# Performance work log

Measured on AMD Instinct MI355X. Metric: run time of the kernel, lower is better.

The kernel has to match this reference:

```python
import jax, jax.numpy as jnp
import numpy as np

D_MODEL, N, L_MAX, BATCH = 512, 64, 2048, 8


def _make_s4_buffers(n):
    # HiPPO-NPLR: hippo[i,j] = sqrt(2i+1)sqrt(2j+1) if i>j; i+1 if i==j (1-indexed)
    i = np.arange(1, n + 1)
    row = np.sqrt(2 * i + 1.0)
    hippo = np.tril(np.outer(row, row), -1) + np.diag(i + 1.0)
    p = 0.5 * np.sqrt(2 * i + 1.0)
    q = 2.0 * p
    S = -hippo + np.outer(p, q)
    lam, V = np.linalg.eig(S)
    Vc = V.conj().T
    return Vc @ p, Vc @ q, lam  # complex128 -> cast to complex64 later


def setup_inputs() -> dict:
    key = jax.random.key(0)
    k1, k2, k3, k4 = jax.random.split(key, 4)
    xavier_std = float(np.sqrt(2.0 / (N + D_MODEL)))
    p, q, lam = _make_s4_buffers(N)
    u = jax.random.normal(k1, (BATCH, L_MAX, D_MODEL), jnp.float32)
    B = jax.random.normal(k2, (D_MODEL, N), jnp.float32) * xavier_std
    Ct = jax.random.normal(k3, (D_MODEL, N), jnp.float32) * xavier_std
    D = jnp.ones((D_MODEL,), jnp.float32)
    log_step = (jax.random.uniform(k4, (D_MODEL,), jnp.float32)
                * (np.log(0.1) - np.log(0.001)) + np.log(0.001))
    return {
        "u": u, "B": B, "Ct": Ct, "D": D, "log_step": log_step,
        "p": jnp.asarray(p, jnp.complex64),
        "q": jnp.asarray(q, jnp.complex64),
        "lam": jnp.asarray(lam, jnp.complex64),
    }


def _s4_forward(u, B, Ct, D, log_step, p, q, lam):
    L = u.shape[1]  # l_max
    omega = jnp.exp((2j * np.pi / L) * jnp.arange(L)).astype(jnp.complex64)  # (L,)
    step = jnp.exp(log_step)                                                 # (d,)
    g = (2.0 / step)[:, None] * ((1.0 - omega) / (1.0 + omega))[None, :]     # (d, L)
    c = 2.0 / (1.0 + omega)                                                  # (L,)
    Bc = B.astype(jnp.complex64)
    Ctc = Ct.astype(jnp.complex64)  # Ct is real -> conj is identity
    v00 = Ctc * Bc                              # (d, n)
    v01 = Ctc * p[None, :]                      # (d, n)
    v10 = jnp.conj(q)[None, :] * Bc             # (d, n)
    v11 = jnp.broadcast_to(jnp.conj(q) * p, v00.shape)
    V = jnp.stack([v00, v01, v10, v11], 0)      # (4, d, n)
    # fused Cauchy reduction: k[k,d,l] = sum_n V[k,d,n] / (g[d,l] - lam[n])
    recip = 1.0 / (g[:, :, None] - lam[None, None, :])  # (d, L, n) big intermediate
    k00, k01, k10, k11 = jnp.einsum('kdn,dln->kdl', V, recip)
    at_roots = c * (k00 - k01 * k10 / (1.0 + k11))      # (d, L)
    # ifft + index reversal (i -> (L - i) mod L), keep real part
    order = (L - jnp.arange(L)) % L
    K = jnp.fft.ifft(at_roots, n=L, axis=-1)[:, order].real.astype(jnp.float32)  # (d, L)
    # non-circular convolution via length-2L FFT
    ud = jnp.fft.rfft(jnp.pad(u, ((0, 0), (0, L), (0, 0))), axis=1)   # (B, L+1, d)
    Kd = jnp.fft.rfft(jnp.pad(K, ((0, 0), (0, L))), axis=-1)          # (d, L+1)
    y = jnp.fft.irfft(jnp.swapaxes(ud, 1, 2) * Kd[None], axis=-1)[..., :L]  # (B, d, L)
    return jnp.swapaxes(y, 1, 2) + D[None, None, :] * u


def reference(u, B, Ct, D, log_step, p, q, lam):
    return _s4_forward(u, B, Ct, D, log_step, p, q, lam)
```

## Files before the change

kernel.cpp:

```cpp
#include <hip/hip_runtime.h>
#include <math.h>

#define D_MODEL 512
#define NSTATE  64
#define LSEQ    2048
#define L2X     4096
#define NBATCH  8
#define NT      512

#define SQ2H 0.70710678118654752f

__device__ __forceinline__ float2 cmulf(float2 a, float2 b) {
    return make_float2(a.x * b.x - a.y * b.y, a.x * b.y + a.y * b.x);
}
__device__ __forceinline__ float2 cmulc(float2 a, float2 w) {
    return make_float2(a.x * w.x + a.y * w.y, a.y * w.x - a.x * w.y);
}
__device__ __forceinline__ float2 cadd(float2 a, float2 b) { return make_float2(a.x + b.x, a.y + b.y); }
__device__ __forceinline__ float2 csub(float2 a, float2 b) { return make_float2(a.x - b.x, a.y - b.y); }
__device__ __forceinline__ float rcpf(float x) { return __builtin_amdgcn_rcpf(x); }
__device__ __forceinline__ float2 cdiv_fast(float2 a, float2 b) {
    float inv = rcpf(b.x * b.x + b.y * b.y);
    return make_float2((a.x * b.x + a.y * b.y) * inv, (a.y * b.x - a.x * b.y) * inv);
}
__device__ __forceinline__ int finitef(float v) {
    return (v == v) && (v < 3.0e38f) && (v > -3.0e38f);
}
__device__ __forceinline__ int octrev12(int x) {
    return ((x & 7) << 9) | ((x & 0x38) << 3) | ((x >> 3) & 0x38) | ((x >> 9) & 7);
}

__device__ __forceinline__ int tidx(int i) { return i + (i >> 4); }
__device__ __forceinline__ int kswz(int i) { return i ^ (i >> 6); }

#define TW_SZ  1088
#define BUF_SZ 4352

__device__ __forceinline__ float2 twget4(const float2* tw, int k) {
    float2 w = tw[tidx(k & 1023)];
    if (k & 1024) w = make_float2(w.y, -w.x);
    if (k & 2048) w = make_float2(-w.x, -w.y);
    return w;
}
#define A4096 (-1.5339807878856412e-3f)
__device__ __forceinline__ void build_tw(float2* tw) {
    for (int k = threadIdx.x; k < 1024; k += NT) {
        float s, c;
        sincosf(A4096 * (float)k, &s, &c);
        tw[tidx(k)] = make_float2(c, s);
    }
}

__device__ __forceinline__ float2 ldc(const float* f, int n, int mode) {
    if (mode == 0) return make_float2(f[n], 0.0f);
    if (mode == 1) return make_float2(f[n], f[64 + n]);
    return make_float2(f[2 * n], f[2 * n + 1]);
}

__device__ __forceinline__ void dft4f(float2 a, float2 b, float2 c, float2 d, float2* F) {
    float2 t0 = cadd(a, c), t1 = csub(a, c);
    float2 t2 = cadd(b, d), t3 = csub(b, d);
    F[0] = cadd(t0, t2);
    F[1] = make_float2(t1.x + t3.y, t1.y - t3.x);
    F[2] = csub(t0, t2);
    F[3] = make_float2(t1.x - t3.y, t1.y + t3.x);
}
__device__ __forceinline__ void dft4i(float2 a, float2 b, float2 c, float2 d, float2* F) {
    float2 t0 = cadd(a, c), t1 = csub(a, c);
    float2 t2 = cadd(b, d), t3 = csub(b, d);
    F[0] = cadd(t0, t2);
    F[1] = make_float2(t1.x - t3.y, t1.y + t3.x);
    F[2] = csub(t0, t2);
    F[3] = make_float2(t1.x + t3.y, t1.y - t3.x);
}
__device__ __forceinline__ void dft8f(const float2* a, float2* X) {
    float2 E[4], O[4];
    dft4f(a[0], a[2], a[4], a[6], E);
    dft4f(a[1], a[3], a[5], a[7], O);
    float2 o1 = make_float2(SQ2H * (O[1].x + O[1].y), SQ2H * (O[1].y - O[1].x));
    float2 o2 = make_float2(O[2].y, -O[2].x);
    float2 o3 = make_float2(SQ2H * (O[3].y - O[3].x), -SQ2H * (O[3].x + O[3].y));
    X[0] = cadd(E[0], O[0]); X[4] = csub(E[0], O[0]);
    X[1] = cadd(E[1], o1);   X[5] = csub(E[1], o1);
    X[2] = cadd(E[2], o2);   X[6] = csub(E[2], o2);
    X[3] = cadd(E[3], o3);   X[7] = csub(E[3], o3);
}
__device__ __forceinline__ void dft8i(const float2* a, float2* X) {
    float2 E[4], O[4];
    dft4i(a[0], a[2], a[4], a[6], E);
    dft4i(a[1], a[3], a[5], a[7], O);
    float2 o1 = make_float2(SQ2H * (O[1].x - O[1].y), SQ2H * (O[1].y + O[1].x));
    float2 o2 = make_float2(-O[2].y, O[2].x);
    float2 o3 = make_float2(-SQ2H * (O[3].x + O[3].y), SQ2H * (O[3].x - O[3].y));
    X[0] = cadd(E[0], O[0]); X[4] = csub(E[0], O[0]);
    X[1] = cadd(E[1], o1);   X[5] = csub(E[1], o1);
    X[2] = cadd(E[2], o2);   X[6] = csub(E[2], o2);
    X[3] = cadd(E[3], o3);   X[7] = csub(E[3], o3);
}

template<int H, int F, int TWMODE, int NBF>
__device__ __forceinline__ void r8_dif_stage(float2* buf, const float2* tw, const float2* twp) {
    __syncthreads();
    const int tid = threadIdx.x;
    if (NBF >= NT || tid < NBF) {
        const int j = tid & (H - 1);
        const int i0 = ((tid - j) << 3) + j;
        float2 a[8], X[8];
        #pragma unroll
        for (int k = 0; k < 8; k++) a[k] = buf[tidx(i0 + k * H)];
        dft8f(a, X);
        if (TWMODE == 1) {
            #pragma unroll
            for (int m = 1; m < 8; m++) X[m] = cmulf(X[m], twp[(m - 1) * H + j]);
        } else if (TWMODE == 2) {
            #pragma unroll
            for (int m = 1; m < 8; m++) X[m] = cmulf(X[m], twget4(tw, (j * F * m) & 4095));
        }
        #pragma unroll
        for (int m = 0; m < 8; m++) buf[tidx(i0 + m * H)] = X[m];
    }
}
template<int H, int F, int TWMODE>
__device__ __forceinline__ void r8_dit_stage(float2* buf, const float2* tw, const float2* twp) {
    __syncthreads();
    const int tid = threadIdx.x;
    const int j = tid & (H - 1);
    const int i0 = ((tid - j) << 3) + j;
    float2 a[8], X[8];
    a[0] = buf[tidx(i0)];
    if (TWMODE == 1) {
        #pragma unroll
        for (int k = 1; k < 8; k++) a[k] = cmulc(buf[tidx(i0 + k * H)], twp[(k - 1) * H + j]);
    } else if (TWMODE == 2) {
        #pragma unroll
        for (int k = 1; k < 8; k++) a[k] = cmulc(buf[tidx(i0 + k * H)], twget4(tw, (j * F * k) & 4095));
    } else {
        #pragma unroll
        for (int k = 1; k < 8; k++) a[k] = buf[tidx(i0 + k * H)];
    }
    dft8i(a, X);
    #pragma unroll
    for (int m = 0; m < 8; m++) buf[tidx(i0 + m * H)] = X[m];
}
__device__ __forceinline__ void r4_dif_h1(float2* buf) {
    __syncthreads();
    const int tid = threadIdx.x;
    const int i0 = tid << 2;
    float2 F[4];
    dft4f(buf[tidx(i0)], buf[tidx(i0 + 1)], buf[tidx(i0 + 2)], buf[tidx(i0 + 3)], F);
    #pragma unroll
    for (int m = 0; m < 4; m++) buf[tidx(i0 + m)] = F[m];
}

__global__ __launch_bounds__(NT) void s4_khat_kernel(
    const float* __restrict__ Bmat, const float* __restrict__ Ct,
    const float* __restrict__ log_step,
    const float* __restrict__ pf, const float* __restrict__ qf,
    const float* __restrict__ lf,
    float2* __restrict__ Khat, int size_hint)
{
    __shared__ float2 tw[TW_SZ];
    __shared__ float2 buf[BUF_SZ];
    __shared__ float2 stash[289];
    __shared__ float  kf[2048];
    __shared__ float2 twS2[448];
    __shared__ float2 twS3[56];
    __shared__ float2 twK2[224];
    __shared__ float2 twK3[28];
    const int d = blockIdx.x;
    const int tid = threadIdx.x;

    build_tw(tw);
    for (int i = tid; i < 448; i += NT) {
        int m = (i >> 6) + 1, j = i & 63; float s, c;
        sincosf(A4096 * (float)(8 * j * m), &s, &c);
        twS2[i] = make_float2(c, s);
    }
    if (tid < 224) { int m = (tid >> 5) + 1, j = tid & 31; float s, c;
        sincosf(A4096 * (float)(16 * j * m), &s, &c); twK2[tid] = make_float2(c, s); }
    else if (tid < 280) { int r = tid - 224; int m = (r >> 3) + 1, j = r & 7; float s, c;
        sincosf(A4096 * (float)(64 * j * m), &s, &c); twS3[r] = make_float2(c, s); }
    else if (tid < 308) { int r = tid - 280; int m = (r >> 2) + 1, j = r & 3; float s, c;
        sincosf(A4096 * (float)(128 * j * m), &s, &c); twK3[r] = make_float2(c, s); }

    int mode;
    if (size_hint >= 128) {
        mode = (fabsf(lf[1] + 0.5f) < 0.05f) ? 1 : 2;
    } else {
        float s1 = 0.0f, s2 = 0.0f;
        bool ok = true;
        for (int n = 0; n < 64; n++) {
            float v = lf[64 + n];
            if (!finitef(v)) { ok = false; break; }
            s1 += v; s2 += fabsf(v);
        }
        mode = (ok && s2 > 0.5f && s2 < 1.0e6f && fabsf(s1) < 1.0e-2f * s2) ? 1 : 0;
    }

    float2* v01  = stash;
    float2* v10  = stash + 64;
    float2* v11  = stash + 128;
    float2* lamS = stash + 192;
    float*  v00  = (float*)(stash + 256);

    if (tid < NSTATE) {
        int n = tid;
        float Bdn = Bmat[d * NSTATE + n];
        float Cdn = Ct[d * NSTATE + n];
        float2 pn = ldc(pf, n, mode);
        float2 qn = ldc(qf, n, mode);
        float2 qc = make_float2(qn.x, -qn.y);
        v00[n]  = Cdn * Bdn;
        v01[n]  = make_float2(Cdn * pn.x, Cdn * pn.y);
        v10[n]  = make_float2(qc.x * Bdn, qc.y * Bdn);
        v11[n]  = cmulf(qc, pn);
        lamS[n] = ldc(lf, n, mode);
    }
    const float two_over_step = 2.0f / expf(log_step[d]);
    __syncthreads();

    float gyr[2], tanl[2];
    float2 a00[2], a01[2], a10[2], a11[2];
    #pragma unroll
    for (int i = 0; i < 2; i++) {
        int l = tid + i * NT;
        float2 w = twget4(tw, 2 * l);
        float cth = w.x, sth = -w.y;
        float tl = sth * rcpf(1.0f + cth);
        tanl[i] = tl;
        gyr[i]  = -two_over_step * tl;
        a00[i] = make_float2(0.f, 0.f); a01[i] = make_float2(0.f, 0.f);
        a10[i] = make_float2(0.f, 0.f); a11[i] = make_float2(0.f, 0.f);
    }
    for (int n = 0; n < NSTATE; n++) {
        float2 ln = lamS[n];
        float  c0 = v00[n];
        float2 c1 = v01[n], c2 = v10[n], c3 = v11[n];
        float dxn = -ln.x;
        float dx2 = ln.x * ln.x;
        #pragma unroll
        for (int i = 0; i < 2; i++) {
            float dy = gyr[i] - ln.y;
            float ir = rcpf(fmaf(dy, dy, dx2));
            float rx = dxn * ir, ry = -dy * ir;
            a00[i].x += c0 * rx;               a00[i].y += c0 * ry;
            a01[i].x += c1.x * rx - c1.y * ry; a01[i].y += c1.x * ry + c1.y * rx;
            a10[i].x += c2.x * rx - c2.y * ry; a10[i].y += c2.x * ry + c2.y * rx;
            a11[i].x += c3.x * rx - c3.y * ry; a11[i].y += c3.x * ry + c3.y * rx;
        }
    }
    __syncthreads();
    #pragma unroll
    for (int i = 0; i < 2; i++) {
        int l = tid + i * NT;
        float2 cl = make_float2(1.0f, -tanl[i]);
        float2 onep = make_float2(1.0f + a11[i].x, a11[i].y);
        float2 corr = cdiv_fast(cmulf(a01[i], a10[i]), onep);
        float2 ar = cmulf(cl, csub(a00[i], corr));
        if (!finitef(ar.x) || !finitef(ar.y)) ar = make_float2(0.0f, 0.0f);
        buf[tidx(l)] = ar;
        if (l > 0) buf[tidx(2048 - l)] = make_float2(ar.x, -ar.y);
    }
    if (tid == 0) buf[tidx(1024)] = make_float2(0.0f, 0.0f);

    r8_dif_stage<256, 2, 2, 256>(buf, tw, nullptr);
    r8_dif_stage<32, 0, 1, 256>(buf, tw, twK2);
    r8_dif_stage<4, 0, 1, 256>(buf, tw, twK3);
    r4_dif_h1(buf);
    __syncthreads();

    const float inv2048 = 1.0f / 2048.0f;
    #pragma unroll
    for (int i = 0; i < 4; i++) {
        int p = tid + i * NT;
        int t = (p >> 8) | (((p >> 5) & 7) << 3) | (((p >> 2) & 7) << 6) | ((p & 3) << 9);
        kf[kswz(t)] = buf[tidx(p)].x * inv2048;
    }
    __syncthreads();

    {
        const float a = kf[kswz(tid)];
        const float b = kf[kswz(tid + 512)];
        const float c = kf[kswz(tid + 1024)];
        const float dd = kf[kswz(tid + 1536)];
        float t0 = a + c, t1 = a - c, t2 = b + dd, t3 = b - dd;
        float2 Xe0 = make_float2(t0 + t2, 0.0f);
        float2 Xe1 = make_float2(t1, -t3);
        float2 Xe2 = make_float2(t0 - t2, 0.0f);
        float2 Xe3 = make_float2(t1, t3);
        float2 y0 = make_float2(a, 0.0f);
        float2 y1 = make_float2(SQ2H * b, -SQ2H * b);
        float2 y2 = make_float2(0.0f, -c);
        float2 y3 = make_float2(-SQ2H * dd, -SQ2H * dd);
        float2 G[4];
        dft4f(y0, y1, y2, y3, G);
        buf[tidx(tid)]        = Xe0;
        buf[tidx(tid + 512)]  = cmulf(G[0], twget4(tw, tid));
        buf[tidx(tid + 1024)] = cmulf(Xe1, twget4(tw, 2 * tid));
        buf[tidx(tid + 1536)] = cmulf(G[1], twget4(tw, (3 * tid) & 4095));
        buf[tidx(tid + 2048)] = cmulf(Xe2, twget4(tw, (4 * tid) & 4095));
        buf[tidx(tid + 2560)] = cmulf(G[2], twget4(tw, (5 * tid) & 4095));
        buf[tidx(tid + 3072)] = cmulf(Xe3, twget4(tw, (6 * tid) & 4095));
        buf[tidx(tid + 3584)] = cmulf(G[3], twget4(tw, (7 * tid) & 4095));
    }
    r8_dif_stage<64, 0, 1, 512>(buf, tw, twS2);
    r8_dif_stage<8, 0, 1, 512>(buf, tw, twS3);
    r8_dif_stage<1, 512, 0, 512>(buf, tw, nullptr);
    __syncthreads();

    const float inv4096 = 1.0f / 4096.0f;
    for (int k = tid; k < L2X; k += NT) {
        float2 v = buf[tidx(k)];
        float vx = v.x * inv4096, vy = v.y * inv4096;
        if (!finitef(vx)) vx = 0.0f;
        if (!finitef(vy)) vy = 0.0f;
        Khat[(size_t)d * L2X + k] = make_float2(vx, vy);
    }
}

__global__ __launch_bounds__(NT) void conv_kernel(
    const float* __restrict__ u, const float2* __restrict__ Khat,
    const float* __restrict__ Dvec, float* __restrict__ out)
{
    __shared__ float2 tw[TW_SZ];
    __shared__ float2 buf[BUF_SZ];
    __shared__ float2 twS2[448];
    __shared__ float2 twS3[56];
    const int blk = blockIdx.x;
    const int d0 = blk >> 3;
    const int bb = blk & 7;
    const int tid = threadIdx.x;

    build_tw(tw);
    for (int i = tid; i < 448; i += NT) {
        int m = (i >> 6) + 1, j = i & 63; float s, c;
        sincosf(A4096 * (float)(8 * j * m), &s, &c);
        twS2[i] = make_float2(c, s);
    }
    if (tid < 56) { int m = (tid >> 3) + 1, j = tid & 7; float s, c;
        sincosf(A4096 * (float)(64 * j * m), &s, &c); twS3[tid] = make_float2(c, s); }

    float2 ureg[4];
    #pragma unroll
    for (int i = 0; i < 4; i++) {
        int t = tid + i * NT;
        ureg[i] = *(const float2*)(u + ((size_t)bb * LSEQ + t) * D_MODEL + 2 * d0);
    }
    __syncthreads();

    {
        float2 Xe[4], G[4];
        dft4f(ureg[0], ureg[1], ureg[2], ureg[3], Xe);
        float2 y1 = make_float2(SQ2H * (ureg[1].x + ureg[1].y), SQ2H * (ureg[1].y - ureg[1].x));
        float2 y2 = make_float2(ureg[2].y, -ureg[2].x);
        float2 y3 = make_float2(SQ2H * (ureg[3].y - ureg[3].x), -SQ2H * (ureg[3].x + ureg[3].y));
        dft4f(ureg[0], y1, y2, y3, G);
        buf[tidx(tid)]        = Xe[0];
        buf[tidx(tid + 512)]  = cmulf(G[0], twget4(tw, tid));
        buf[tidx(tid + 1024)] = cmulf(Xe[1], twget4(tw, 2 * tid));
        buf[tidx(tid + 1536)] = cmulf(G[1], twget4(tw, (3 * tid) & 4095));
        buf[tidx(tid + 2048)] = cmulf(Xe[2], twget4(tw, (4 * tid) & 4095));
        buf[tidx(tid + 2560)] = cmulf(G[2], twget4(tw, (5 * tid) & 4095));
        buf[tidx(tid + 3072)] = cmulf(Xe[3], twget4(tw, (6 * tid) & 4095));
        buf[tidx(tid + 3584)] = cmulf(G[3], twget4(tw, (7 * tid) & 4095));
    }
    r8_dif_stage<64, 0, 1, 512>(buf, tw, twS2);
    r8_dif_stage<8, 0, 1, 512>(buf, tw, twS3);
    r8_dif_stage<1, 512, 0, 512>(buf, tw, nullptr);
    __syncthreads();

    const float2* K0 = Khat + (size_t)(2 * d0) * L2X;
    const float2* K1 = K0 + L2X;
    for (int t0 = tid; t0 < L2X; t0 += NT) {
        int fr = octrev12(t0);
        int jm = octrev12((L2X - fr) & (L2X - 1));
        if (t0 > jm) continue;
        float2 Zk = buf[tidx(t0)], Zm = buf[tidx(jm)];
        float2 U0 = make_float2(0.5f * (Zk.x + Zm.x), 0.5f * (Zk.y - Zm.y));
        float2 U1 = make_float2(0.5f * (Zk.y + Zm.y), 0.5f * (Zm.x - Zk.x));
        float2 Y0 = cmulf(U0, K0[t0]);
        float2 Y1 = cmulf(U1, K1[t0]);
        buf[tidx(t0)] = make_float2(Y0.x - Y1.y, Y0.y + Y1.x);
        buf[tidx(jm)] = make_float2(Y0.x + Y1.y, Y1.x - Y0.y);
    }

    r8_dit_stage<1, 512, 0>(buf, tw, nullptr);
    r8_dit_stage<8, 64, 1>(buf, tw, twS3);
    r8_dit_stage<64, 8, 1>(buf, tw, twS2);
    __syncthreads();

    const float dv0 = Dvec[2 * d0];
    const float dv1 = Dvec[2 * d0 + 1];
    {
        float2 c0 = buf[tidx(tid)];
        float2 c1 = cmulc(buf[tidx(tid +  512)], twget4(tw, tid));
        float2 c2 = cmulc(buf[tidx(tid + 1024)], twget4(tw, 2 * tid));
        float2 c3 = cmulc(buf[tidx(tid + 1536)], twget4(tw, (3 * tid) & 4095));
        float2 c4 = cmulc(buf[tidx(tid + 2048)], twget4(tw, (4 * tid) & 4095));
        float2 c5 = cmulc(buf[tidx(tid + 2560)], twget4(tw, (5 * tid) & 4095));
        float2 c6 = cmulc(buf[tidx(tid + 3072)], twget4(tw, (6 * tid) & 4095));
        float2 c7 = cmulc(buf[tidx(tid + 3584)], twget4(tw, (7 * tid) & 4095));
        float2 E[4], O[4];
        dft4i(c0, c2, c4, c6, E);
        dft4i(c1, c3, c5, c7, O);
        float2 o1 = make_float2(SQ2H * (O[1].x - O[1].y), SQ2H * (O[1].y + O[1].x));
        float2 o2 = make_float2(-O[2].y, O[2].x);
        float2 o3 = make_float2(-SQ2H * (O[3].x + O[3].y), SQ2H * (O[3].x - O[3].y));
        float2 y[4];
        y[0] = cadd(E[0], O[0]);
        y[1] = cadd(E[1], o1);
        y[2] = cadd(E[2], o2);
        y[3] = cadd(E[3], o3);
        #pragma unroll
        for (int m = 0; m < 4; m++) {
            int t = tid + 512 * m;
            float o0 = y[m].x + dv0 * ureg[m].x;
            float o1f = y[m].y + dv1 * ureg[m].y;
            if (!finitef(o0)) o0 = 4.0e5f;
            if (!finitef(o1f)) o1f = 4.0e5f;
            *(float2*)(out + ((size_t)bb * LSEQ + t) * D_MODEL + 2 * d0) = make_float2(o0, o1f);
        }
    }
}

extern "C" void kernel_launch(void* const* d_in, const int* in_sizes, int n_in,
                              void* d_out, int out_size, void* d_ws, size_t ws_size,
                              hipStream_t stream) {
    (void)n_in; (void)out_size; (void)ws_size;
    const float* u        = (const float*)d_in[0];
    const float* Bmat     = (const float*)d_in[1];
    const float* Ct       = (const float*)d_in[2];
    const float* Dvec     = (const float*)d_in[3];
    const float* log_step = (const float*)d_in[4];
    const float* pf       = (const float*)d_in[5];
    const float* qf       = (const float*)d_in[6];
    const float* lf       = (const float*)d_in[7];
    float* out = (float*)d_out;

    int size_hint = in_sizes[5];

    float2* Khat = (float2*)d_ws;

    s4_khat_kernel<<<D_MODEL, NT, 0, stream>>>(Bmat, Ct, log_step, pf, qf, lf, Khat, size_hint);
    conv_kernel<<<NBATCH * (D_MODEL / 2), NT, 0, stream>>>(u, Khat, Dvec, out);
}
```

Measured before the change: 177.0 us.

## Switch 4096-point FFTs to radix-16 with two batch rows per block

Replaces the radix-8 FFT stages (a first pass plus three radix-8 passes over 512 threads) with radix-16 passes, where 256 threads handle one 4096-point transform. This cuts the number of stages and barriers and keeps more butterfly work in registers. The convolution kernel now processes two batch rows per block, each in its own half of the block with a separate shared buffer, so it launches half as many blocks. The Khat kernel's forward FFT is rewritten the same way and now reuses the main buffer instead of a separate kf array. In exchange, the conv kernel needs roughly double the shared memory per block and more registers per thread, which may reduce occupancy.

```diff
diff --git a/kernel.cpp b/kernel.cpp
--- a/kernel.cpp
+++ b/kernel.cpp
@@ -9,6 +9,9 @@
 #define NT      512
 
 #define SQ2H 0.70710678118654752f
+#define C16  0.92387953251128674f
+#define S16  0.38268343236508977f
+#define A4096 (-1.5339807878856412e-3f)
 
 __device__ __forceinline__ float2 cmulf(float2 a, float2 b) {
     return make_float2(a.x * b.x - a.y * b.y, a.x * b.y + a.y * b.x);
@@ -26,8 +29,8 @@
 __device__ __forceinline__ int finitef(float v) {
     return (v == v) && (v < 3.0e38f) && (v > -3.0e38f);
 }
-__device__ __forceinline__ int octrev12(int x) {
-    return ((x & 7) << 9) | ((x & 0x38) << 3) | ((x >> 3) & 0x38) | ((x >> 9) & 7);
+__device__ __forceinline__ int hexrev12(int x) {
+    return ((x & 15) << 8) | (x & 240) | ((x >> 8) & 15);
 }
 
 __device__ __forceinline__ int tidx(int i) { return i + (i >> 4); }
@@ -42,7 +45,6 @@
     if (k & 2048) w = make_float2(-w.x, -w.y);
     return w;
 }
-#define A4096 (-1.5339807878856412e-3f)
 __device__ __forceinline__ void build_tw(float2* tw) {
     for (int k = threadIdx.x; k < 1024; k += NT) {
         float s, c;
@@ -97,6 +99,87 @@
     X[2] = cadd(E[2], o2);   X[6] = csub(E[2], o2);
     X[3] = cadd(E[3], o3);   X[7] = csub(E[3], o3);
 }
+__device__ __forceinline__ void dft16f(const float2* a, float2* X) {
+    float2 ev[8], od[8], E[8], O[8];
+    #pragma unroll
+    for (int r = 0; r < 8; r++) { ev[r] = a[2 * r]; od[r] = a[2 * r + 1]; }
+    dft8f(ev, E); dft8f(od, O);
+    float2 t0 = O[0];
+    float2 t1 = cmulf(O[1], make_float2(C16, -S16));
+    float2 t2 = make_float2(SQ2H * (O[2].x + O[2].y), SQ2H * (O[2].y - O[2].x));
+    float2 t3 = cmulf(O[3], make_float2(S16, -C16));
+    float2 t4 = make_float2(O[4].y, -O[4].x);
+    float2 t5 = cmulf(O[5], make_float2(-S16, -C16));
+    float2 t6 = make_float2(SQ2H * (O[6].y - O[6].x), -SQ2H * (O[6].x + O[6].y));
+    float2 t7 = cmulf(O[7], make_float2(-C16, -S16));
+    X[0] = cadd(E[0], t0); X[8]  = csub(E[0], t0);
+    X[1] = cadd(E[1], t1); X[9]  = csub(E[1], t1);
+    X[2] = cadd(E[2], t2); X[10] = csub(E[2], t2);
+    X[3] = cadd(E[3], t3); X[11] = csub(E[3], t3);
+    X[4] = cadd(E[4], t4); X[12] = csub(E[4], t4);
+    X[5] = cadd(E[5], t5); X[13] = csub(E[5], t5);
+    X[6] = cadd(E[6], t6); X[14] = csub(E[6], t6);
+    X[7] = cadd(E[7], t7); X[15] = csub(E[7], t7);
+}
+__device__ __forceinline__ void dft16i(const float2* a, float2* X) {
+    float2 ev[8], od[8], E[8], O[8];
+    #pragma unroll
+    for (int r = 0; r < 8; r++) { ev[r] = a[2 * r]; od[r] = a[2 * r + 1]; }
+    dft8i(ev, E); dft8i(od, O);
+    float2 t0 = O[0];
+    float2 t1 = cmulf(O[1], make_float2(C16, S16));
+    float2 t2 = make_float2(SQ2H * (O[2].x - O[2].y), SQ2H * (O[2].x + O[2].y));
+    float2 t3 = cmulf(O[3], make_float2(S16, C16));
+    float2 t4 = make_float2(-O[4].y, O[4].x);
+    float2 t5 = cmulf(O[5], make_float2(-S16, C16));
+    float2 t6 = make_float2(-SQ2H * (O[6].x + O[6].y), SQ2H * (O[6].x - O[6].y));
+    float2 t7 = cmulf(O[7], make_float2(-C16, S16));
+    X[0] = cadd(E[0], t0); X[8]  = csub(E[0], t0);
+    X[1] = cadd(E[1], t1); X[9]  = csub(E[1], t1);
+    X[2] = cadd(E[2], t2); X[10] = csub(E[2], t2);
+    X[3] = cadd(E[3], t3); X[11] = csub(E[3], t3);
+    X[4] = cadd(E[4], t4); X[12] = csub(E[4], t4);
+    X[5] = cadd(E[5], t5); X[13] = csub(E[5], t5);
+    X[6] = cadd(E[6], t6); X[14] = csub(E[6], t6);
+    X[7] = cadd(E[7], t7); X[15] = csub(E[7], t7);
+}
+
+template<int H, bool TW>
+__device__ __forceinline__ void r16_dif_ld(float2* buf, const float2* twp, int t) {
+    const int j = t & (H - 1);
+    const int i0 = ((t - j) << 4) + j;
+    const int base = i0 + (i0 >> 4);
+    constexpr int S = (H >= 16) ? (H + (H >> 4)) : 1;
+    float2 a[16], X[16];
+    #pragma unroll
+    for (int k = 0; k < 16; k++) a[k] = buf[base + k * S];
+    dft16f(a, X);
+    buf[base] = X[0];
+    #pragma unroll
+    for (int m = 1; m < 16; m++) {
+        float2 v = X[m];
+        if (TW) v = cmulf(v, twp[(m - 1) * 16 + j]);
+        buf[base + m * S] = v;
+    }
+}
+template<int H, bool TW>
+__device__ __forceinline__ void r16_dit_ld(float2* buf, const float2* twp, int t) {
+    const int j = t & (H - 1);
+    const int i0 = ((t - j) << 4) + j;
+    const int base = i0 + (i0 >> 4);
+    constexpr int S = (H >= 16) ? (H + (H >> 4)) : 1;
+    float2 a[16], X[16];
+    a[0] = buf[base];
+    #pragma unroll
+    for (int k = 1; k < 16; k++) {
+        float2 v = buf[base + k * S];
+        if (TW) v = cmulc(v, twp[(k - 1) * 16 + j]);
+        a[k] = v;
+    }
+    dft16i(a, X);
+    #pragma unroll
+    for (int m = 0; m < 16; m++) buf[base + m * S] = X[m];
+}
 
 template<int H, int F, int TWMODE, int NBF>
 __device__ __forceinline__ void r8_dif_stage(float2* buf, const float2* tw, const float2* twp) {
@@ -119,28 +202,6 @@
         #pragma unroll
         for (int m = 0; m < 8; m++) buf[tidx(i0 + m * H)] = X[m];
     }
-}
-template<int H, int F, int TWMODE>
-__device__ __forceinline__ void r8_dit_stage(float2* buf, const float2* tw, const float2* twp) {
-    __syncthreads();
-    const int tid = threadIdx.x;
-    const int j = tid & (H - 1);
-    const int i0 = ((tid - j) << 3) + j;
-    float2 a[8], X[8];
-    a[0] = buf[tidx(i0)];
-    if (TWMODE == 1) {
-        #pragma unroll
-        for (int k = 1; k < 8; k++) a[k] = cmulc(buf[tidx(i0 + k * H)], twp[(k - 1) * H + j]);
-    } else if (TWMODE == 2) {
-        #pragma unroll
-        for (int k = 1; k < 8; k++) a[k] = cmulc(buf[tidx(i0 + k * H)], twget4(tw, (j * F * k) & 4095));
-    } else {
-        #pragma unroll
-        for (int k = 1; k < 8; k++) a[k] = buf[tidx(i0 + k * H)];
-    }
-    dft8i(a, X);
-    #pragma unroll
-    for (int m = 0; m < 8; m++) buf[tidx(i0 + m * H)] = X[m];
 }
 __device__ __forceinline__ void r4_dif_h1(float2* buf) {
     __syncthreads();
@@ -162,26 +223,19 @@
     __shared__ float2 tw[TW_SZ];
     __shared__ float2 buf[BUF_SZ];
     __shared__ float2 stash[289];
-    __shared__ float  kf[2048];
-    __shared__ float2 twS2[448];
-    __shared__ float2 twS3[56];
     __shared__ float2 twK2[224];
     __shared__ float2 twK3[28];
+    __shared__ float2 twp2[240];
     const int d = blockIdx.x;
     const int tid = threadIdx.x;
 
     build_tw(tw);
-    for (int i = tid; i < 448; i += NT) {
-        int m = (i >> 6) + 1, j = i & 63; float s, c;
-        sincosf(A4096 * (float)(8 * j * m), &s, &c);
-        twS2[i] = make_float2(c, s);
-    }
     if (tid < 224) { int m = (tid >> 5) + 1, j = tid & 31; float s, c;
         sincosf(A4096 * (float)(16 * j * m), &s, &c); twK2[tid] = make_float2(c, s); }
-    else if (tid < 280) { int r = tid - 224; int m = (r >> 3) + 1, j = r & 7; float s, c;
-        sincosf(A4096 * (float)(64 * j * m), &s, &c); twS3[r] = make_float2(c, s); }
-    else if (tid < 308) { int r = tid - 280; int m = (r >> 2) + 1, j = r & 3; float s, c;
+    else if (tid < 252) { int r = tid - 224; int m = (r >> 3) + 1, j = r & 7; float s, c;
         sincosf(A4096 * (float)(128 * j * m), &s, &c); twK3[r] = make_float2(c, s); }
+    else if (tid < 492) { int r = tid - 252; int m = (r >> 4) + 1, j = r & 15; float s, c;
+        sincosf(A4096 * (float)(16 * j * m), &s, &c); twp2[r] = make_float2(c, s); }
 
     int mode;
     if (size_hint >= 128) {
@@ -270,42 +324,52 @@
     __syncthreads();
 
     const float inv2048 = 1.0f / 2048.0f;
+    float krv[4]; int tpos[4];
     #pragma unroll
     for (int i = 0; i < 4; i++) {
         int p = tid + i * NT;
-        int t = (p >> 8) | (((p >> 5) & 7) << 3) | (((p >> 2) & 7) << 6) | ((p & 3) << 9);
-        kf[kswz(t)] = buf[tidx(p)].x * inv2048;
-    }
-    __syncthreads();
-
-    {
-        const float a = kf[kswz(tid)];
-        const float b = kf[kswz(tid + 512)];
-        const float c = kf[kswz(tid + 1024)];
-        const float dd = kf[kswz(tid + 1536)];
-        float t0 = a + c, t1 = a - c, t2 = b + dd, t3 = b - dd;
-        float2 Xe0 = make_float2(t0 + t2, 0.0f);
-        float2 Xe1 = make_float2(t1, -t3);
-        float2 Xe2 = make_float2(t0 - t2, 0.0f);
-        float2 Xe3 = make_float2(t1, t3);
-        float2 y0 = make_float2(a, 0.0f);
-        float2 y1 = make_float2(SQ2H * b, -SQ2H * b);
-        float2 y2 = make_float2(0.0f, -c);
-        float2 y3 = make_float2(-SQ2H * dd, -SQ2H * dd);
-        float2 G[4];
-        dft4f(y0, y1, y2, y3, G);
-        buf[tidx(tid)]        = Xe0;
-        buf[tidx(tid + 512)]  = cmulf(G[0], twget4(tw, tid));
-        buf[tidx(tid + 1024)] = cmulf(Xe1, twget4(tw, 2 * tid));
-        buf[tidx(tid + 1536)] = cmulf(G[1], twget4(tw, (3 * tid) & 4095));
-        buf[tidx(tid + 2048)] = cmulf(Xe2, twget4(tw, (4 * tid) & 4095));
-        buf[tidx(tid + 2560)] = cmulf(G[2], twget4(tw, (5 * tid) & 4095));
-        buf[tidx(tid + 3072)] = cmulf(Xe3, twget4(tw, (6 * tid) & 4095));
-        buf[tidx(tid + 3584)] = cmulf(G[3], twget4(tw, (7 * tid) & 4095));
-    }
-    r8_dif_stage<64, 0, 1, 512>(buf, tw, twS2);
-    r8_dif_stage<8, 0, 1, 512>(buf, tw, twS3);
-    r8_dif_stage<1, 512, 0, 512>(buf, tw, nullptr);
+        tpos[i] = (p >> 8) | (((p >> 5) & 7) << 3) | (((p >> 2) & 7) << 6) | ((p & 3) << 9);
+        krv[i] = buf[tidx(p)].x * inv2048;
+    }
+    __syncthreads();
+    float* kfp = (float*)buf;
+    #pragma unroll
+    for (int i = 0; i < 4; i++) kfp[kswz(tpos[i])] = krv[i];
+    __syncthreads();
+
+    float a8[8];
+    if (tid < 256) {
+        #pragma unroll
+        for (int k = 0; k < 8; k++) a8[k] = kfp[kswz(tid + 256 * k)];
+    }
+    __syncthreads();
+    if (tid < 256) {
+        const int j = tid;
+        float2 ar8[8], bq[8], E[8], O[8], X[16];
+        #pragma unroll
+        for (int k = 0; k < 8; k++) ar8[k] = make_float2(a8[k], 0.0f);
+        dft8f(ar8, E);
+        bq[0] = make_float2(a8[0], 0.0f);
+        bq[1] = make_float2(C16 * a8[1], -S16 * a8[1]);
+        bq[2] = make_float2(SQ2H * a8[2], -SQ2H * a8[2]);
+        bq[3] = make_float2(S16 * a8[3], -C16 * a8[3]);
+        bq[4] = make_float2(0.0f, -a8[4]);
+        bq[5] = make_float2(-S16 * a8[5], -C16 * a8[5]);
+        bq[6] = make_float2(-SQ2H * a8[6], -SQ2H * a8[6]);
+        bq[7] = make_float2(-C16 * a8[7], -S16 * a8[7]);
+        dft8f(bq, O);
+        #pragma unroll
+        for (int r = 0; r < 8; r++) { X[2 * r] = E[r]; X[2 * r + 1] = O[r]; }
+        const int base = j + (j >> 4);
+        buf[base] = X[0];
+        #pragma unroll
+        for (int m = 1; m < 16; m++)
+            buf[base + 272 * m] = cmulf(X[m], twget4(tw, j * m));
+    }
+    __syncthreads();
+    if (tid < 256) r16_dif_ld<16, true>(buf, twp2, tid);
+    __syncthreads();
+    if (tid < 256) r16_dif_ld<1, false>(buf, nullptr, tid);
     __syncthreads();
 
     const float inv4096 = 1.0f / 4096.0f;
@@ -323,57 +387,60 @@
     const float* __restrict__ Dvec, float* __restrict__ out)
 {
     __shared__ float2 tw[TW_SZ];
-    __shared__ float2 buf[BUF_SZ];
-    __shared__ float2 twS2[448];
-    __shared__ float2 twS3[56];
+    __shared__ float2 bufs[2 * BUF_SZ];
+    __shared__ float2 twp2[240];
     const int blk = blockIdx.x;
-    const int d0 = blk >> 3;
-    const int bb = blk & 7;
+    const int d0 = blk >> 2;
+    const int bp = blk & 3;
     const int tid = threadIdx.x;
+    const int half = tid >> 8;
+    const int jj = tid & 255;
+    const int b = bp * 2 + half;
+    float2* buf = bufs + half * BUF_SZ;
 
     build_tw(tw);
-    for (int i = tid; i < 448; i += NT) {
-        int m = (i >> 6) + 1, j = i & 63; float s, c;
-        sincosf(A4096 * (float)(8 * j * m), &s, &c);
-        twS2[i] = make_float2(c, s);
-    }
-    if (tid < 56) { int m = (tid >> 3) + 1, j = tid & 7; float s, c;
-        sincosf(A4096 * (float)(64 * j * m), &s, &c); twS3[tid] = make_float2(c, s); }
-
-    float2 ureg[4];
-    #pragma unroll
-    for (int i = 0; i < 4; i++) {
-        int t = tid + i * NT;
-        ureg[i] = *(const float2*)(u + ((size_t)bb * LSEQ + t) * D_MODEL + 2 * d0);
-    }
+    if (tid < 240) { int m = (tid >> 4) + 1, j = tid & 15; float s, c;
+        sincosf(A4096 * (float)(16 * j * m), &s, &c); twp2[tid] = make_float2(c, s); }
+
+    const float* ub = u + (size_t)b * LSEQ * D_MODEL + 2 * d0;
+    float2 ureg[8];
+    #pragma unroll
+    for (int k = 0; k < 8; k++)
+        ureg[k] = *(const float2*)(ub + (size_t)(jj + 256 * k) * D_MODEL);
+
     __syncthreads();
 
     {
-        float2 Xe[4], G[4];
-        dft4f(ureg[0], ureg[1], ureg[2], ureg[3], Xe);
-        float2 y1 = make_float2(SQ2H * (ureg[1].x + ureg[1].y), SQ2H * (ureg[1].y - ureg[1].x));
-        float2 y2 = make_float2(ureg[2].y, -ureg[2].x);
-        float2 y3 = make_float2(SQ2H * (ureg[3].y - ureg[3].x), -SQ2H * (ureg[3].x + ureg[3].y));
-        dft4f(ureg[0], y1, y2, y3, G);
-        buf[tidx(tid)]        = Xe[0];
-        buf[tidx(tid + 512)]  = cmulf(G[0], twget4(tw, tid));
-        buf[tidx(tid + 1024)] = cmulf(Xe[1], twget4(tw, 2 * tid));
-        buf[tidx(tid + 1536)] = cmulf(G[1], twget4(tw, (3 * tid) & 4095));
-        buf[tidx(tid + 2048)] = cmulf(Xe[2], twget4(tw, (4 * tid) & 4095));
-        buf[tidx(tid + 2560)] = cmulf(G[2], twget4(tw, (5 * tid) & 4095));
-        buf[tidx(tid + 3072)] = cmulf(Xe[3], twget4(tw, (6 * tid) & 4095));
-        buf[tidx(tid + 3584)] = cmulf(G[3], twget4(tw, (7 * tid) & 4095));
-    }
-    r8_dif_stage<64, 0, 1, 512>(buf, tw, twS2);
-    r8_dif_stage<8, 0, 1, 512>(buf, tw, twS3);
-    r8_dif_stage<1, 512, 0, 512>(buf, tw, nullptr);
+        float2 E[8], O[8], bq[8], X[16];
+        dft8f(ureg, E);
+        bq[0] = ureg[0];
+        bq[1] = cmulf(ureg[1], make_float2(C16, -S16));
+        bq[2] = make_float2(SQ2H * (ureg[2].x + ureg[2].y), SQ2H * (ureg[2].y - ureg[2].x));
+        bq[3] = cmulf(ureg[3], make_float2(S16, -C16));
+        bq[4] = make_float2(ureg[4].y, -ureg[4].x);
+        bq[5] = cmulf(ureg[5], make_float2(-S16, -C16));
+        bq[6] = make_float2(SQ2H * (ureg[6].y - ureg[6].x), -SQ2H * (ureg[6].x + ureg[6].y));
+        bq[7] = cmulf(ureg[7], make_float2(-C16, -S16));
+        dft8f(bq, O);
+        #pragma unroll
+        for (int r = 0; r < 8; r++) { X[2 * r] = E[r]; X[2 * r + 1] = O[r]; }
+        const int base = jj + (jj >> 4);
+        buf[base] = X[0];
+        #pragma unroll
+        for (int m = 1; m < 16; m++)
+            buf[base + 272 * m] = cmulf(X[m], twget4(tw, jj * m));
+    }
+    __syncthreads();
+    r16_dif_ld<16, true>(buf, twp2, jj);
+    __syncthreads();
+    r16_dif_ld<1, false>(buf, nullptr, jj);
     __syncthreads();
 
     const float2* K0 = Khat + (size_t)(2 * d0) * L2X;
     const float2* K1 = K0 + L2X;
-    for (int t0 = tid; t0 < L2X; t0 += NT) {
-        int fr = octrev12(t0);
-        int jm = octrev12((L2X - fr) & (L2X - 1));
+    for (int t0 = jj; t0 < L2X; t0 += 256) {
+        int fr = hexrev12(t0);
+        int jm = hexrev12((L2X - fr) & (L2X - 1));
         if (t0 > jm) continue;
         float2 Zk = buf[tidx(t0)], Zm = buf[tidx(jm)];
         float2 U0 = make_float2(0.5f * (Zk.x + Zm.x), 0.5f * (Zk.y - Zm.y));
@@ -383,42 +450,42 @@
         buf[tidx(t0)] = make_float2(Y0.x - Y1.y, Y0.y + Y1.x);
         buf[tidx(jm)] = make_float2(Y0.x + Y1.y, Y1.x - Y0.y);
     }
-
-    r8_dit_stage<1, 512, 0>(buf, tw, nullptr);
-    r8_dit_stage<8, 64, 1>(buf, tw, twS3);
-    r8_dit_stage<64, 8, 1>(buf, tw, twS2);
+    __syncthreads();
+    r16_dit_ld<1, false>(buf, nullptr, jj);
+    __syncthreads();
+    r16_dit_ld<16, true>(buf, twp2, jj);
     __syncthreads();
 
     const float dv0 = Dvec[2 * d0];
     const float dv1 = Dvec[2 * d0 + 1];
     {
-        float2 c0 = buf[tidx(tid)];
-        float2 c1 = cmulc(buf[tidx(tid +  512)], twget4(tw, tid));
-        float2 c2 = cmulc(buf[tidx(tid + 1024)], twget4(tw, 2 * tid));
-        float2 c3 = cmulc(buf[tidx(tid + 1536)], twget4(tw, (3 * tid) & 4095));
-        float2 c4 = cmulc(buf[tidx(tid + 2048)], twget4(tw, (4 * tid) & 4095));
-        float2 c5 = cmulc(buf[tidx(tid + 2560)], twget4(tw, (5 * tid) & 4095));
-        float2 c6 = cmulc(buf[tidx(tid + 3072)], twget4(tw, (6 * tid) & 4095));
-        float2 c7 = cmulc(buf[tidx(tid + 3584)], twget4(tw, (7 * tid) & 4095));
-        float2 E[4], O[4];
-        dft4i(c0, c2, c4, c6, E);
-        dft4i(c1, c3, c5, c7, O);
-        float2 o1 = make_float2(SQ2H * (O[1].x - O[1].y), SQ2H * (O[1].y + O[1].x));
-        float2 o2 = make_float2(-O[2].y, O[2].x);
-        float2 o3 = make_float2(-SQ2H * (O[3].x + O[3].y), SQ2H * (O[3].x - O[3].y));
-        float2 y[4];
-        y[0] = cadd(E[0], O[0]);
-        y[1] = cadd(E[1], o1);
-        y[2] = cadd(E[2], o2);
-        y[3] = cadd(E[3], o3);
-        #pragma unroll
-        for (int m = 0; m < 4; m++) {
-            int t = tid + 512 * m;
-            float o0 = y[m].x + dv0 * ureg[m].x;
-            float o1f = y[m].y + dv1 * ureg[m].y;
+        const int base = jj + (jj >> 4);
+        float2 a[16];
+        a[0] = buf[base];
+        #pragma unroll
+        for (int k = 1; k < 16; k++)
+            a[k] = cmulc(buf[base + 272 * k], twget4(tw, jj * k));
+        float2 ev[8], od[8], E[8], O[8];
+        #pragma unroll
+        for (int r = 0; r < 8; r++) { ev[r] = a[2 * r]; od[r] = a[2 * r + 1]; }
+        dft8i(ev, E); dft8i(od, O);
+        float2 t[8];
+        t[0] = O[0];
+        t[1] = cmulf(O[1], make_float2(C16, S16));
+        t[2] = make_float2(SQ2H * (O[2].x - O[2].y), SQ2H * (O[2].x + O[2].y));
+        t[3] = cmulf(O[3], make_float2(S16, C16));
+        t[4] = make_float2(-O[4].y, O[4].x);
+        t[5] = cmulf(O[5], make_float2(-S16, C16));
+        t[6] = make_float2(-SQ2H * (O[6].x + O[6].y), SQ2H * (O[6].x - O[6].y));
+        t[7] = cmulf(O[7], make_float2(-C16, S16));
+        #pragma unroll
+        for (int m = 0; m < 8; m++) {
+            float2 y = cadd(E[m], t[m]);
+            float o0 = y.x + dv0 * ureg[m].x;
+            float o1 = y.y + dv1 * ureg[m].y;
             if (!finitef(o0)) o0 = 4.0e5f;
-            if (!finitef(o1f)) o1f = 4.0e5f;
-            *(float2*)(out + ((size_t)bb * LSEQ + t) * D_MODEL + 2 * d0) = make_float2(o0, o1f);
+            if (!finitef(o1)) o1 = 4.0e5f;
+            *(float2*)(out + ((size_t)b * LSEQ + jj + 256 * m) * D_MODEL + 2 * d0) = make_float2(o0, o1);
         }
     }
 }
@@ -442,5 +509,5 @@
     float2* Khat = (float2*)d_ws;
 
     s4_khat_kernel<<<D_MODEL, NT, 0, stream>>>(Bmat, Ct, log_step, pf, qf, lf, Khat, size_hint);
-    conv_kernel<<<NBATCH * (D_MODEL / 2), NT, 0, stream>>>(u, Khat, Dvec, out);
-}
+    conv_kernel<<<NBATCH * (D_MODEL / 4), NT, 0, stream>>>(u, Khat, Dvec, out);
+}
```

After: 184.5 us. 4.3% more time.

## Compute Khat via even/odd split, reusing spectrum for even bins and 2048-point FFT

Applied to the files above, without the earlier changes.

Replaces the zero-padded 4096-point forward FFT of the kernel with an even/odd decomposition. The even bins are written straight from the already-known spectrum at the roots, scaled and conjugated. The odd bins come from a 2048-point FFT of the twiddle-modulated kernel that reuses the existing 2048-point stage pipeline. This drops the extra shared-memory arrays and their twiddle tables, which cuts LDS use and some setup work, at the cost of scattered global writes in octal-bit-reversed order.

```diff
diff --git a/kernel.cpp b/kernel.cpp
--- a/kernel.cpp
+++ b/kernel.cpp
@@ -9,6 +9,7 @@
 #define NT      512
 
 #define SQ2H 0.70710678118654752f
+#define A4096 (-1.5339807878856412e-3f)
 
 __device__ __forceinline__ float2 cmulf(float2 a, float2 b) {
     return make_float2(a.x * b.x - a.y * b.y, a.x * b.y + a.y * b.x);
@@ -29,6 +30,9 @@
 __device__ __forceinline__ int octrev12(int x) {
     return ((x & 7) << 9) | ((x & 0x38) << 3) | ((x >> 3) & 0x38) | ((x >> 9) & 7);
 }
+__device__ __forceinline__ int rev8884(int q) {
+    return (q >> 8) | (((q >> 5) & 7) << 3) | (((q >> 2) & 7) << 6) | ((q & 3) << 9);
+}
 
 __device__ __forceinline__ int tidx(int i) { return i + (i >> 4); }
 __device__ __forceinline__ int kswz(int i) { return i ^ (i >> 6); }
@@ -42,7 +46,6 @@
     if (k & 2048) w = make_float2(-w.x, -w.y);
     return w;
 }
-#define A4096 (-1.5339807878856412e-3f)
 __device__ __forceinline__ void build_tw(float2* tw) {
     for (int k = threadIdx.x; k < 1024; k += NT) {
         float s, c;
@@ -162,25 +165,17 @@
     __shared__ float2 tw[TW_SZ];
     __shared__ float2 buf[BUF_SZ];
     __shared__ float2 stash[289];
-    __shared__ float  kf[2048];
-    __shared__ float2 twS2[448];
-    __shared__ float2 twS3[56];
     __shared__ float2 twK2[224];
     __shared__ float2 twK3[28];
     const int d = blockIdx.x;
     const int tid = threadIdx.x;
+    const float inv4096 = 1.0f / 4096.0f;
+    float2* Kd = Khat + (size_t)d * L2X;
 
     build_tw(tw);
-    for (int i = tid; i < 448; i += NT) {
-        int m = (i >> 6) + 1, j = i & 63; float s, c;
-        sincosf(A4096 * (float)(8 * j * m), &s, &c);
-        twS2[i] = make_float2(c, s);
-    }
     if (tid < 224) { int m = (tid >> 5) + 1, j = tid & 31; float s, c;
         sincosf(A4096 * (float)(16 * j * m), &s, &c); twK2[tid] = make_float2(c, s); }
-    else if (tid < 280) { int r = tid - 224; int m = (r >> 3) + 1, j = r & 7; float s, c;
-        sincosf(A4096 * (float)(64 * j * m), &s, &c); twS3[r] = make_float2(c, s); }
-    else if (tid < 308) { int r = tid - 280; int m = (r >> 2) + 1, j = r & 3; float s, c;
+    else if (tid < 252) { int r = tid - 224; int m = (r >> 3) + 1, j = r & 7; float s, c;
         sincosf(A4096 * (float)(128 * j * m), &s, &c); twK3[r] = make_float2(c, s); }
 
     int mode;
@@ -260,8 +255,17 @@
         if (!finitef(ar.x) || !finitef(ar.y)) ar = make_float2(0.0f, 0.0f);
         buf[tidx(l)] = ar;
         if (l > 0) buf[tidx(2048 - l)] = make_float2(ar.x, -ar.y);
-    }
-    if (tid == 0) buf[tidx(1024)] = make_float2(0.0f, 0.0f);
+        if (l == 0) {
+            Kd[0] = make_float2(ar.x * inv4096, 0.0f);
+        } else {
+            Kd[octrev12(2 * l)] = make_float2(ar.x * inv4096, -ar.y * inv4096);
+            Kd[octrev12(4096 - 2 * l)] = make_float2(ar.x * inv4096, ar.y * inv4096);
+        }
+    }
+    if (tid == 0) {
+        buf[tidx(1024)] = make_float2(0.0f, 0.0f);
+        Kd[octrev12(2048)] = make_float2(0.0f, 0.0f);
+    }
 
     r8_dif_stage<256, 2, 2, 256>(buf, tw, nullptr);
     r8_dif_stage<32, 0, 1, 256>(buf, tw, twK2);
@@ -270,51 +274,49 @@
     __syncthreads();
 
     const float inv2048 = 1.0f / 2048.0f;
+    float krv[4]; int tpos[4];
     #pragma unroll
     for (int i = 0; i < 4; i++) {
         int p = tid + i * NT;
-        int t = (p >> 8) | (((p >> 5) & 7) << 3) | (((p >> 2) & 7) << 6) | ((p & 3) << 9);
-        kf[kswz(t)] = buf[tidx(p)].x * inv2048;
-    }
-    __syncthreads();
-
-    {
-        const float a = kf[kswz(tid)];
-        const float b = kf[kswz(tid + 512)];
-        const float c = kf[kswz(tid + 1024)];
-        const float dd = kf[kswz(tid + 1536)];
-        float t0 = a + c, t1 = a - c, t2 = b + dd, t3 = b - dd;
-        float2 Xe0 = make_float2(t0 + t2, 0.0f);
-        float2 Xe1 = make_float2(t1, -t3);
-        float2 Xe2 = make_float2(t0 - t2, 0.0f);
-        float2 Xe3 = make_float2(t1, t3);
-        float2 y0 = make_float2(a, 0.0f);
-        float2 y1 = make_float2(SQ2H * b, -SQ2H * b);
-        float2 y2 = make_float2(0.0f, -c);
-        float2 y3 = make_float2(-SQ2H * dd, -SQ2H * dd);
-        float2 G[4];
-        dft4f(y0, y1, y2, y3, G);
-        buf[tidx(tid)]        = Xe0;
-        buf[tidx(tid + 512)]  = cmulf(G[0], twget4(tw, tid));
-        buf[tidx(tid + 1024)] = cmulf(Xe1, twget4(tw, 2 * tid));
-        buf[tidx(tid + 1536)] = cmulf(G[1], twget4(tw, (3 * tid) & 4095));
-        buf[tidx(tid + 2048)] = cmulf(Xe2, twget4(tw, (4 * tid) & 4095));
-        buf[tidx(tid + 2560)] = cmulf(G[2], twget4(tw, (5 * tid) & 4095));
-        buf[tidx(tid + 3072)] = cmulf(Xe3, twget4(tw, (6 * tid) & 4095));
-        buf[tidx(tid + 3584)] = cmulf(G[3], twget4(tw, (7 * tid) & 4095));
-    }
-    r8_dif_stage<64, 0, 1, 512>(buf, tw, twS2);
-    r8_dif_stage<8, 0, 1, 512>(buf, tw, twS3);
-    r8_dif_stage<1, 512, 0, 512>(buf, tw, nullptr);
-    __syncthreads();
-
-    const float inv4096 = 1.0f / 4096.0f;
-    for (int k = tid; k < L2X; k += NT) {
-        float2 v = buf[tidx(k)];
+        tpos[i] = rev8884(p);
+        krv[i] = buf[tidx(p)].x * inv2048;
+    }
+    __syncthreads();
+    float* kfp = (float*)buf;
+    #pragma unroll
+    for (int i = 0; i < 4; i++) kfp[kswz(tpos[i])] = krv[i];
+    __syncthreads();
+
+    float2 md[4];
+    #pragma unroll
+    for (int i = 0; i < 4; i++) {
+        int t = tid + i * NT;
+        float kv = kfp[kswz(t)];
+        float2 w = twget4(tw, t);
+        md[i] = make_float2(kv * w.x, kv * w.y);
+    }
+    __syncthreads();
+    #pragma unroll
+    for (int i = 0; i < 4; i++) {
+        int t = tid + i * NT;
+        buf[tidx(t)] = md[i];
+    }
+
+    r8_dif_stage<256, 2, 2, 256>(buf, tw, nullptr);
+    r8_dif_stage<32, 0, 1, 256>(buf, tw, twK2);
+    r8_dif_stage<4, 0, 1, 256>(buf, tw, twK3);
+    r4_dif_h1(buf);
+    __syncthreads();
+
+    #pragma unroll
+    for (int i = 0; i < 4; i++) {
+        int q = tid + i * NT;
+        int j = rev8884(q);
+        float2 v = buf[tidx(q)];
         float vx = v.x * inv4096, vy = v.y * inv4096;
         if (!finitef(vx)) vx = 0.0f;
         if (!finitef(vy)) vy = 0.0f;
-        Khat[(size_t)d * L2X + k] = make_float2(vx, vy);
+        Kd[octrev12(2 * j + 1)] = make_float2(vx, vy);
     }
 }
 
```

Result: no change. 178.5 us (+0.8%).
